# Kernel optimization log

Hardware: AMD Instinct MI355X
Metric: run time of the kernel (lower is better)

The kernel has to match this reference:

```python
import jax, jax.numpy as jnp
import numpy as np
from jax import lax

V, D, H, B, S = 30000, 300, 300, 512, 100
DA, WIND1, HOPS, NC = 100, 40, 3, 7


def setup_inputs() -> dict:
    key = jax.random.key(0)
    ks = iter(jax.random.split(key, 64))
    def w(shape, fan_in):
        return jax.random.normal(next(ks), shape, jnp.float32) / np.float32(np.sqrt(fan_in))
    inp = {}
    inp["sents"] = jax.random.randint(next(ks), (B, S), 0, V)
    inp["lengths"] = jax.random.randint(next(ks), (B,), 1, S + 1)
    inp["emb"] = w((V, D), D)
    for d in ("f", "b"):
        inp["lstm_Wih_" + d] = w((4 * H, D), D)
        inp["lstm_Whh_" + d] = w((4 * H, H), H)
        inp["lstm_bih_" + d] = w((4 * H,), H)
        inp["lstm_bhh_" + d] = w((4 * H,), H)
        inp["gru_Wih_" + d] = w((3 * DA, DA), DA)
        inp["gru_Whh_" + d] = w((3 * DA, DA), DA)
        inp["gru_bih_" + d] = w((3 * DA,), DA)
        inp["gru_bhh_" + d] = w((3 * DA,), DA)
    inp["lin1_W"] = w((DA, 2 * H), 2 * H)
    inp["lin1_b"] = w((DA,), 2 * H)
    for nm in ("att_Wr", "att_Ur", "att_W", "att_U"):
        inp[nm] = w((HOPS, DA, DA), DA)
    for nm in ("att_br", "att_bur", "att_bw", "att_bu"):
        inp[nm] = w((HOPS, DA), DA)
    inp["cls_W"] = w((NC, DA), DA)
    inp["cls_b"] = w((NC,), DA)
    return inp


def _lstm_dir(x_tm, m_tm, Wih, Whh, bih, bhh):
    # x_tm: [S,B,D], m_tm: [S,B,1] bool. Masked scan == pack_padded semantics
    xg = jnp.einsum('sbd,gd->sbg', x_tm, Wih) + bih  # precompute input gates [S,B,4H]
    Hh = Whh.shape[1]
    def step(carry, inp):
        h, c = carry
        xgt, mt = inp
        g = xgt + h @ Whh.T + bhh
        i, f, gg, o = jnp.split(g, 4, -1)  # torch LSTM gate order i,f,g,o
        cn = jax.nn.sigmoid(f) * c + jax.nn.sigmoid(i) * jnp.tanh(gg)
        hn = jax.nn.sigmoid(o) * jnp.tanh(cn)
        return (jnp.where(mt, hn, h), jnp.where(mt, cn, c)), jnp.where(mt, hn, 0.0)
    init = (jnp.zeros((x_tm.shape[1], Hh), x_tm.dtype), jnp.zeros((x_tm.shape[1], Hh), x_tm.dtype))
    _, out = lax.scan(step, init, (xg, m_tm))
    return out


def _gru_dir(x_tm, Wih, Whh, bih, bhh):
    xg = jnp.einsum('sbd,gd->sbg', x_tm, Wih) + bih  # [S,B,3H]
    Hh = Whh.shape[1]
    def step(h, xgt):
        hg = h @ Whh.T + bhh
        xr, xz, xn = jnp.split(xgt, 3, -1)
        hr, hz, hn = jnp.split(hg, 3, -1)
        r = jax.nn.sigmoid(xr + hr)
        z = jax.nn.sigmoid(xz + hz)
        n = jnp.tanh(xn + r * hn)
        h2 = (1.0 - z) * n + z * h
        return h2, h2
    _, out = lax.scan(step, jnp.zeros((x_tm.shape[1], Hh), x_tm.dtype), xg)
    return out


def _attgru(mem_tm, gates_tm, Wr, br, Ur, bur, W, bw, U, bu):
    # mem_tm: [W,B-1,100], gates_tm: [W,B-1,1]; AttnGRUCell recurrence
    cr = jnp.einsum('sbd,hd->sbh', mem_tm, Wr) + br
    cw = jnp.einsum('sbd,hd->sbh', mem_tm, W) + bw
    def step(h, inp):
        crt, cwt, g = inp
        r = jax.nn.sigmoid(crt + h @ Ur.T + bur)
        ht = jnp.tanh(cwt + r * (h @ U.T + bu))
        return g * ht + (1.0 - g) * h, None
    h0 = jnp.zeros((mem_tm.shape[1], Wr.shape[0]), mem_tm.dtype)
    h, _ = lax.scan(step, h0, (cr, cw, gates_tm))
    return h  # [B-1,100]


def reference(sents, lengths, emb,
              lstm_Wih_f, lstm_Whh_f, lstm_bih_f, lstm_bhh_f,
              lstm_Wih_b, lstm_Whh_b, lstm_bih_b, lstm_bhh_b,
              lin1_W, lin1_b,
              gru_Wih_f, gru_Whh_f, gru_bih_f, gru_bhh_f,
              gru_Wih_b, gru_Whh_b, gru_bih_b, gru_bhh_b,
              att_Wr, att_br, att_Ur, att_bur, att_W, att_bw, att_U, att_bu,
              cls_W, cls_b):
    we = emb[sents]  # [B,S,D]
    mask = jnp.arange(S)[None, :] < lengths[:, None]  # [B,S]
    x_tm = we.transpose(1, 0, 2)
    m_tm = mask.T[:, :, None]
    out_f = _lstm_dir(x_tm, m_tm, lstm_Wih_f, lstm_Whh_f, lstm_bih_f, lstm_bhh_f)
    out_b = jnp.flip(_lstm_dir(jnp.flip(x_tm, 0), jnp.flip(m_tm, 0),
                               lstm_Wih_b, lstm_Whh_b, lstm_bih_b, lstm_bhh_b), 0)
    w_gru = jnp.concatenate([out_f, out_b], -1).transpose(1, 0, 2)  # [B,S,2H], 0 at pads
    maxpl = jnp.max(w_gru, axis=1)
    s_utt = jnp.tanh(maxpl @ lin1_W.T + lin1_b)  # [B,100]; dropout = eval identity
    # context window: slot j of query i holds utterance i-WIND1+j (zero-padded front)
    idx = jnp.arange(1, B)[:, None] - WIND1 + jnp.arange(WIND1)[None, :]  # [B-1,W]
    valid = idx >= 0
    bt = s_utt[jnp.clip(idx, 0)] * valid[..., None].astype(s_utt.dtype)  # [B-1,W,100]
    bt_tm = bt.transpose(1, 0, 2)  # [W,B-1,100]
    mem_f = _gru_dir(bt_tm, gru_Wih_f, gru_Whh_f, gru_bih_f, gru_bhh_f)
    mem_b = jnp.flip(_gru_dir(jnp.flip(bt_tm, 0), gru_Wih_b, gru_Whh_b, gru_bih_b, gru_bhh_b), 0)
    mem_tm = bt_tm + mem_f + mem_b  # fusion: input + fwd + bwd GRU states
    mem_bank = mem_tm.transpose(1, 0, 2)  # [B-1,W,100]
    eps = s_utt[1:][:, None, :]  # query [B-1,1,100]
    attn_ws = []
    for hop in range(HOPS):
        attn = jnp.einsum('bqd,bkd->bqk', eps, mem_bank)  # [B-1,1,W]
        attn = jnp.where(valid[:, None, :], attn, -1e10)
        scores = jax.nn.softmax(attn, -1)
        gates_tm = scores[:, 0, :].T[:, :, None]  # [W,B-1,1]
        h = _attgru(mem_tm, gates_tm, att_Wr[hop], att_br[hop], att_Ur[hop], att_bur[hop],
                    att_W[hop], att_bw[hop], att_U[hop], att_bu[hop])
        eps = eps + h[:, None, :]
        attn_ws.append(scores[:, 0, :])
    s_cont = jnp.concatenate([s_utt[:1], eps[:, 0, :]], 0)  # [B,100]
    pred = jax.nn.log_softmax(s_cont @ cls_W.T + cls_b, -1)  # [B,NC]
    return pred, jnp.stack(attn_ws)  # attn weights [HOPS,B-1,W]
```

## Files before the change

### kernel.cpp

```cpp
#include <hip/hip_runtime.h>
#include <cstdint>
#include <cstddef>

typedef unsigned short u16;
typedef unsigned int   u32;
typedef unsigned long long u64;

#define S_LEN 100
#define B_SZ  512
#define H_LS  300
#define NHOP  3
#define NC_   7
#define BM1   511
#define NBD3  60

using bf16x8 = __attribute__((ext_vector_type(8))) short;
using f32x4  = __attribute__((ext_vector_type(4))) float;

__device__ __forceinline__ float u2f(u16 u) {
  union { u32 i; float f; } x; x.i = ((u32)u) << 16; return x.f;
}
__device__ __forceinline__ u16 f2u(float f) {
  u32 bits = __float_as_uint(f);
  bits += 0x7fffu + ((bits >> 16) & 1u);
  return (u16)(bits >> 16);
}
__device__ __forceinline__ float sigm(float x) { return 1.0f / (1.0f + expf(-x)); }

__global__ void detect_k(const u32* __restrict__ raw, int* __restrict__ flag) {
  __shared__ int cnt;
  if (threadIdx.x == 0) cnt = 0;
  __syncthreads();
  u32 w = raw[threadIdx.x];
  u32 lo = w & 0xFFFFu;
  int e = (int)((lo >> 7) & 0xFF);
  int pl = (lo == 0u || (e >= 0x70 && e <= 0x8E)) ? 1 : 0;
  atomicAdd(&cnt, pl);
  __syncthreads();
  if (threadIdx.x == 0) *flag = (cnt >= 192) ? 1 : 0;
}

#define NF_NSEG 28
#define NF_TOT  1748007
struct NormFArgs { const void* src[NF_NSEG]; const int* flag; float* dst; };

__global__ __launch_bounds__(256) void norm_f32(NormFArgs a) {
  const int P[NF_NSEG + 1] = {
    0,360000,720000,1080000,1440000,1441200,1442400,1443600,
    1444800,1474800,1504800,1505100,1505400,1535400,1565400,1565700,
    1566000,1626000,1626100,1656100,1686100,1716100,1746100,1746400,
    1746700,1747000,1747300,1748000,1748007};
  int fl = *a.flag;
  int stride = gridDim.x * 256;
  for (int i = blockIdx.x * 256 + threadIdx.x; i < NF_TOT; i += stride) {
    int s = 0;
    while (i >= P[s + 1]) ++s;
    int k = i - P[s];
    float v = fl ? u2f(((const u16*)a.src[s])[k]) : ((const float*)a.src[s])[k];
    a.dst[i] = v;
  }
}
#define AF_LWIH_F 0
#define AF_LWHH_F 360000
#define AF_LWIH_B 720000
#define AF_LWHH_B 1080000
#define AF_LBIH_F 1440000
#define AF_LBHH_F 1441200
#define AF_LBIH_B 1442400
#define AF_LBHH_B 1443600
#define AF_GWIH_F 1444800
#define AF_GWHH_F 1474800
#define AF_GBIH_F 1504800
#define AF_GBHH_F 1505100
#define AF_GWIH_B 1505400
#define AF_GWHH_B 1535400
#define AF_GBIH_B 1565400
#define AF_GBHH_B 1565700
#define AF_LIN1W  1566000
#define AF_LIN1B  1626000
#define AF_ATTWR  1626100
#define AF_ATTUR  1656100
#define AF_ATTW   1686100
#define AF_ATTU   1716100
#define AF_ATTBR  1746100
#define AF_ATTBUR 1746400
#define AF_ATTBW  1746700
#define AF_ATTBU  1747000
#define AF_CLSW   1747300
#define AF_CLSB   1748000

__global__ void transp_k(const float* __restrict__ allf, float* __restrict__ wt) {
  int idx = blockIdx.x * 256 + threadIdx.x;
  if (idx >= 120000) return;
  int seg = idx / 10000;
  int rem = idx - seg * 10000;
  int k = rem / 100, j = rem - (rem / 100) * 100;
  int srcbase;
  if (seg < 3)      srcbase = AF_GWHH_F + seg * 10000;
  else if (seg < 6) srcbase = AF_GWHH_B + (seg - 3) * 10000;
  else if (seg < 9) srcbase = AF_ATTUR + (seg - 6) * 10000;
  else              srcbase = AF_ATTU  + (seg - 9) * 10000;
  wt[seg * 10000 + k * 100 + j] = allf[srcbase + j * 100 + k];
}

__global__ void tr_lstm2(const float* __restrict__ allf, u16* __restrict__ wL2,
                         float* __restrict__ bsum) {
  int idx = blockIdx.x * 256 + threadIdx.x;
  if (idx < 1536000) {
    int dir = idx / 768000;
    int rem = idx - dir * 768000;
    int c = rem / 640, kp = rem - (rem / 640) * 640;
    int j = c >> 2, g = c & 3;
    float v = 0.f;
    if (kp < 320) {
      if (kp < 300)
        v = allf[(dir ? AF_LWIH_B : AF_LWIH_F) + (g * 300 + j) * 300 + kp];
    } else {
      int k2 = kp - 320;
      if (k2 < 300)
        v = allf[(dir ? AF_LWHH_B : AF_LWHH_F) + (g * 300 + j) * 300 + k2];
    }
    wL2[idx] = f2u(v);
  } else if (idx < 1538400) {
    int i2 = idx - 1536000;
    int dir = i2 / 1200, gj = i2 - (i2 / 1200) * 1200;
    bsum[i2] = allf[(dir ? AF_LBIH_B : AF_LBIH_F) + gj]
             + allf[(dir ? AF_LBHH_B : AF_LBHH_F) + gj];
  }
}

__global__ __launch_bounds__(256) void xgat2(const int* __restrict__ sents,
                                             const void* __restrict__ emb,
                                             const int* __restrict__ flag,
                                             u16* __restrict__ xallR) {
  __shared__ int toks[64];
  int tid = threadIdx.x;
  int r0 = blockIdx.x * 64, t = blockIdx.y;
  int fl = *flag;
  if (tid < 64) toks[tid] = sents[(r0 + tid) * S_LEN + t];
  __syncthreads();
  for (int idx = tid; idx < 64 * 320; idx += 256) {
    int r = idx / 320, k = idx - (idx / 320) * 320;
    u16 v = 0;
    if (k < 300) {
      size_t si = (size_t)toks[r] * 300 + k;
      v = fl ? ((const u16*)emb)[si] : f2u(((const float*)emb)[si]);
    }
    xallR[((size_t)t * 512 + r0 + r) * 320 + k] = v;
  }
}

struct Lstm8Args {
  const int* lens;
  const u16* xallR;
  const u16* wL2;
  const float* bsum;
  float* hbufR;
  float* maxb;
  int* cnt;
};

__global__ __launch_bounds__(512, 1) void lstm8(Lstm8Args a) {
  __shared__ u16   WLh[80 * 640];
  __shared__ float Gs[128][84];
  const int tid = threadIdx.x;
  const int r0  = blockIdx.x * 128;
  const int ct  = blockIdx.y;
  const int dir = blockIdx.z;

  {
    const u64* wsrc = (const u64*)(a.wL2 + (size_t)dir * 768000 + (size_t)ct * 80 * 640);
    for (int i = tid; i < 80 * 160; i += 512) {
      int cc = i / 160, kw = i - (i / 160) * 160;
      u64 v = wsrc[(size_t)cc * 160 + kw];
      *(u64*)((char*)WLh + cc * 1280 + ((kw * 8) ^ ((cc & 7) << 4))) = v;
    }
  }

  const int w  = tid >> 6;
  const int l  = tid & 63;
  const int lr = l & 15;
  const int aq = l >> 4;
  const int arow = r0 + w * 16 + lr;

  float cq[5], hq[5], mxv[5], bsv[5][4];
  int lenv[5];
  #pragma unroll
  for (int i = 0; i < 5; ++i) {
    int idx = tid * 5 + i;
    int r = idx / 20, jj = idx - (idx / 20) * 20;
    int j = ct * 20 + jj;
    cq[i] = 0.f; hq[i] = 0.f; mxv[i] = -INFINITY;
    lenv[i] = a.lens[r0 + r];
    #pragma unroll
    for (int g = 0; g < 4; ++g) bsv[i][g] = a.bsum[dir * 1200 + g * 300 + j];
  }

  int* cptr = a.cnt + dir * 16;
  int target = 0;
  __syncthreads();

  for (int s = 0; s < S_LEN; ++s) {
    const int tt  = dir ? (S_LEN - 1 - s) : s;
    const int cur = s & 1, nxt = cur ^ 1;

    f32x4 acc0 = {0,0,0,0}, acc1 = {0,0,0,0}, acc2 = {0,0,0,0},
          acc3 = {0,0,0,0}, acc4 = {0,0,0,0};

    const u16*   xrow = a.xallR + ((size_t)tt * 512 + arow) * 320 + aq * 8;
    const float* hrow = a.hbufR + (((size_t)cur * 2 + dir) * 512 + arow) * 320 + aq * 8;

    for (int ks = 0; ks < 10; ++ks) {
      bf16x8 Af = *(const bf16x8*)(xrow + ks * 32);
      #pragma unroll
      for (int cf = 0; cf < 5; ++cf) {
        int cc = cf * 16 + lr;
        bf16x8 Bf = *(const bf16x8*)((const char*)WLh + cc * 1280 +
                                     ((ks * 64 + aq * 16) ^ ((cc & 7) << 4)));
        f32x4& ac = (cf == 0) ? acc0 : (cf == 1) ? acc1 : (cf == 2) ? acc2
                  : (cf == 3) ? acc3 : acc4;
        ac = __builtin_amdgcn_mfma_f32_16x16x32_bf16(Af, Bf, ac, 0, 0, 0);
      }
    }
    for (int ks = 0; ks < 10; ++ks) {
      const float* hp = hrow + ks * 32;
      float4 h0 = *(const float4*)hp;
      float4 h1 = *(const float4*)(hp + 4);
      union { u32 u[4]; bf16x8 v; } pk;
      pk.u[0] = ((u32)f2u(h0.y) << 16) | (u32)f2u(h0.x);
      pk.u[1] = ((u32)f2u(h0.w) << 16) | (u32)f2u(h0.z);
      pk.u[2] = ((u32)f2u(h1.y) << 16) | (u32)f2u(h1.x);
      pk.u[3] = ((u32)f2u(h1.w) << 16) | (u32)f2u(h1.z);
      bf16x8 Af = pk.v;
      #pragma unroll
      for (int cf = 0; cf < 5; ++cf) {
        int cc = cf * 16 + lr;
        bf16x8 Bf = *(const bf16x8*)((const char*)WLh + cc * 1280 +
                                     (((ks + 10) * 64 + aq * 16) ^ ((cc & 7) << 4)));
        f32x4& ac = (cf == 0) ? acc0 : (cf == 1) ? acc1 : (cf == 2) ? acc2
                  : (cf == 3) ? acc3 : acc4;
        ac = __builtin_amdgcn_mfma_f32_16x16x32_bf16(Af, Bf, ac, 0, 0, 0);
      }
    }

    #pragma unroll
    for (int rr = 0; rr < 4; ++rr) {
      Gs[w * 16 + aq * 4 + rr][0 * 16 + lr] = acc0[rr];
      Gs[w * 16 + aq * 4 + rr][1 * 16 + lr] = acc1[rr];
      Gs[w * 16 + aq * 4 + rr][2 * 16 + lr] = acc2[rr];
      Gs[w * 16 + aq * 4 + rr][3 * 16 + lr] = acc3[rr];
      Gs[w * 16 + aq * 4 + rr][4 * 16 + lr] = acc4[rr];
    }
    __syncthreads();

    #pragma unroll
    for (int i = 0; i < 5; ++i) {
      int idx = tid * 5 + i;
      int r = idx / 20, jj = idx - (idx / 20) * 20;
      bool m = tt < lenv[i];
      float4 g4 = *(const float4*)&Gs[r][jj * 4];
      if (m) {
        float gi = g4.x + bsv[i][0];
        float gf = g4.y + bsv[i][1];
        float gg = g4.z + bsv[i][2];
        float go = g4.w + bsv[i][3];
        cq[i] = sigm(gf) * cq[i] + sigm(gi) * tanhf(gg);
        hq[i] = sigm(go) * tanhf(cq[i]);
        mxv[i] = fmaxf(mxv[i], hq[i]);
      } else {
        mxv[i] = fmaxf(mxv[i], 0.f);
      }
      a.hbufR[(((size_t)nxt * 2 + dir) * 512 + r0 + r) * 320 + ct * 20 + jj] = hq[i];
    }

    target += NBD3;
    __syncthreads();
    if (tid == 0) {
      __threadfence();
      __hip_atomic_fetch_add(cptr, 1, __ATOMIC_ACQ_REL, __HIP_MEMORY_SCOPE_AGENT);
      while (__hip_atomic_load(cptr, __ATOMIC_ACQUIRE, __HIP_MEMORY_SCOPE_AGENT) < target) {
        __builtin_amdgcn_s_sleep(1);
      }
      __threadfence();
    }
    __syncthreads();
  }

  #pragma unroll
  for (int i = 0; i < 5; ++i) {
    int idx = tid * 5 + i;
    int r = idx / 20, jj = idx - (idx / 20) * 20;
    a.maxb[(size_t)(r0 + r) * 600 + dir * 300 + ct * 20 + jj] = mxv[i];
  }
}

__global__ __launch_bounds__(128) void sutt_k(const float* __restrict__ maxb,
                                              const float* __restrict__ W,
                                              const float* __restrict__ bb,
                                              float* __restrict__ sutt) {
  int b = blockIdx.x, tid = threadIdx.x;
  __shared__ float mx[600];
  for (int i = tid; i < 600; i += 128) mx[i] = maxb[b * 600 + i];
  __syncthreads();
  if (tid < 100) {
    float acc = bb[tid];
    const float* wr = W + tid * 600;
    for (int k = 0; k < 600; ++k) acc += mx[k] * wr[k];
    sutt[b * 100 + tid] = tanhf(acc);
  }
}

__global__ __launch_bounds__(256) void gxg3(const float* __restrict__ sutt,
                                            const float* __restrict__ Wf, const float* __restrict__ bf_,
                                            const float* __restrict__ Wb, const float* __restrict__ bb_,
                                            float* __restrict__ xg) {
  __shared__ float bts[32][101];
  int tid = threadIdx.x;
  int rt = blockIdx.x * 32, t = blockIdx.y, dir = blockIdx.z;
  int tin = dir ? (39 - t) : t;
  for (int idx = tid; idx < 3200; idx += 256) {
    int r = idx / 100, k = idx - r * 100, row = rt + r;
    float v = 0.f;
    if (row < BM1) {
      int srow = row + 1 - 40 + tin;
      if (srow >= 0) v = sutt[srow * 100 + k];
    }
    bts[r][k] = v;
  }
  __syncthreads();
  const float* Wm = dir ? Wb : Wf;
  const float* bm = dir ? bb_ : bf_;
  for (int o = tid; o < 9600; o += 256) {
    int r = o & 31, g = o >> 5;
    float acc = bm[g];
    const float* wr = Wm + g * 100;
    const float* br = bts[r];
    for (int k = 0; k < 100; ++k) acc += br[k] * wr[k];
    int row = rt + r;
    if (row < BM1) xg[(((size_t)dir * 40 + t) * BM1 + row) * 300 + g] = acc;
  }
}

struct Gru4Args {
  const float* wt;
  const float* bhh[2];
  const float* xg;
  float* memf; float* memb;
};

__global__ __launch_bounds__(512) void gru4(Gru4Args a) {
  __shared__ float WT[30000];
  __shared__ float hl[2][4][104];
  int tid = threadIdx.x, rt = blockIdx.x * 4, dir = blockIdx.y;
  const float* src = a.wt + dir * 30000;
  for (int i = tid; i < 30000; i += 512) WT[i] = src[i];
  for (int i = tid; i < 832; i += 512) ((float*)hl)[i] = 0.f;
  int r = tid / 100, j = tid - r * 100;
  int row = rt + r;
  bool act = (tid < 400) && (row < BM1);
  const float* bhh = a.bhh[dir];
  float xr = 0.f, xz = 0.f, xn = 0.f;
  if (act) {
    size_t xb = ((size_t)(dir * 40) * BM1 + row) * 300;
    xr = a.xg[xb + j]; xz = a.xg[xb + 100 + j]; xn = a.xg[xb + 200 + j];
  }
  float hprev = 0.f;
  __syncthreads();
  for (int t = 0; t < 40; ++t) {
    int nxt = (t + 1) & 1, cur = t & 1;
    float xr2 = 0.f, xz2 = 0.f, xn2 = 0.f;
    if (act && t < 39) {
      size_t xb = ((size_t)(dir * 40 + t + 1) * BM1 + row) * 300;
      xr2 = a.xg[xb + j]; xz2 = a.xg[xb + 100 + j]; xn2 = a.xg[xb + 200 + j];
    }
    float v = 0.f;
    if (act) {
      float hr = bhh[j], hz = bhh[100 + j], hn = bhh[200 + j];
      const float* w0 = WT + j;
      const float* hrow = hl[cur][r];
      for (int k = 0; k < 100; ++k) {
        float hv = hrow[k];
        hr += hv * w0[k * 100];
        hz += hv * w0[10000 + k * 100];
        hn += hv * w0[20000 + k * 100];
      }
      float rg_ = sigm(xr + hr), zg = sigm(xz + hz);
      float ng = tanhf(xn + rg_ * hn);
      v = (1.f - zg) * ng + zg * hprev;
      int tin = dir ? (39 - t) : t;
      (dir ? a.memb : a.memf)[((size_t)tin * BM1 + row) * 100 + j] = v;
    }
    if (tid < 400) hl[nxt][r][j] = v;
    hprev = v;
    __syncthreads();
    xr = xr2; xz = xz2; xn = xn2;
  }
}

__global__ void memcomb(const float* __restrict__ memf, const float* __restrict__ memb,
                        const float* __restrict__ sutt, float* __restrict__ memm) {
  int idx = blockIdx.x * 256 + threadIdx.x;
  if (idx >= 40 * BM1 * 100) return;
  int j = idx % 100; int rem = idx / 100; int row = rem % BM1; int t = rem / BM1;
  float v = memf[idx] + memb[idx];
  int sidx = row + 1 - 40 + t;
  if (sidx >= 0) v += sutt[sidx * 100 + j];
  memm[idx] = v;
}

__global__ void epsinit(const float* __restrict__ sutt, float* __restrict__ eps) {
  int idx = blockIdx.x * 256 + threadIdx.x;
  if (idx < BM1 * 100) eps[idx] = sutt[idx + 100];
}

__global__ __launch_bounds__(64) void attnsc(const float* __restrict__ eps,
                                             const float* __restrict__ memm,
                                             float* __restrict__ gatesw,
                                             float* __restrict__ outat) {
  int row = blockIdx.x, k = threadIdx.x;
  __shared__ float el[100];
  for (int i = k; i < 100; i += 64) el[i] = eps[row * 100 + i];
  __syncthreads();
  float val = -INFINITY;
  if (k < 40) {
    if (row + 1 - 40 + k >= 0) {
      const float* mrow = memm + ((size_t)k * BM1 + row) * 100;
      float s = 0.f;
      for (int d = 0; d < 100; ++d) s += el[d] * mrow[d];
      val = s;
    } else val = -1e10f;
  }
  float mx = val;
  for (int off = 32; off > 0; off >>= 1) mx = fmaxf(mx, __shfl_xor(mx, off));
  float ex = (k < 40) ? expf(val - mx) : 0.f;
  float sm = ex;
  for (int off = 32; off > 0; off >>= 1) sm += __shfl_xor(sm, off);
  if (k < 40) {
    float sc = ex / sm;
    gatesw[k * BM1 + row] = sc;
    outat[row * 40 + k] = sc;
  }
}

__global__ __launch_bounds__(256) void crcw3(const float* __restrict__ memm,
                                             const float* __restrict__ Wr, const float* __restrict__ br,
                                             const float* __restrict__ Ww, const float* __restrict__ bw,
                                             float* __restrict__ crb, float* __restrict__ cwb) {
  __shared__ float ml[32][101];
  int tid = threadIdx.x;
  int rt = blockIdx.x * 32, t = blockIdx.y, which = blockIdx.z;
  for (int idx = tid; idx < 3200; idx += 256) {
    int r = idx / 100, k = idx - r * 100; int row = rt + r;
    ml[r][k] = (row < BM1) ? memm[((size_t)t * BM1 + row) * 100 + k] : 0.f;
  }
  __syncthreads();
  const float* Wm = which ? Ww : Wr;
  const float* bm = which ? bw : br;
  float* ob = which ? cwb : crb;
  for (int o = tid; o < 3200; o += 256) {
    int r = o & 31, hh = o >> 5;
    float acc = bm[hh];
    const float* wr = Wm + hh * 100;
    for (int k = 0; k < 100; ++k) acc += ml[r][k] * wr[k];
    int row = rt + r;
    if (row < BM1) ob[((size_t)t * BM1 + row) * 100 + hh] = acc;
  }
}

struct Att4Args {
  const float* urT; const float* uT;
  const float* bur; const float* bu;
  const float* crb; const float* cwb;
  const float* gatesw; float* eps;
};

__global__ __launch_bounds__(512) void attscan4(Att4Args a) {
  __shared__ float UrT[10000];
  __shared__ float UT[10000];
  __shared__ float hl[2][4][104];
  int tid = threadIdx.x, rt = blockIdx.x * 4;
  for (int i = tid; i < 10000; i += 512) { UrT[i] = a.urT[i]; UT[i] = a.uT[i]; }
  for (int i = tid; i < 832; i += 512) ((float*)hl)[i] = 0.f;
  int r = tid / 100, j = tid - r * 100;
  int row = rt + r;
  bool act = (tid < 400) && (row < BM1);
  float cr = 0.f, cw = 0.f, gw = 0.f;
  if (act) {
    size_t ix = (size_t)row * 100 + j;
    cr = a.crb[ix]; cw = a.cwb[ix]; gw = a.gatesw[row];
  }
  float hprev = 0.f;
  __syncthreads();
  for (int t = 0; t < 40; ++t) {
    int nxt = (t + 1) & 1, cur = t & 1;
    float cr2 = 0.f, cw2 = 0.f, gw2 = 0.f;
    if (act && t < 39) {
      size_t ix = ((size_t)(t + 1) * BM1 + row) * 100 + j;
      cr2 = a.crb[ix]; cw2 = a.cwb[ix]; gw2 = a.gatesw[(t + 1) * BM1 + row];
    }
    float v = 0.f;
    if (act) {
      float hr = a.bur[j], hu = a.bu[j];
      const float* hrow = hl[cur][r];
      for (int k = 0; k < 100; ++k) {
        float hv = hrow[k];
        hr += hv * UrT[k * 100 + j];
        hu += hv * UT[k * 100 + j];
      }
      float rg_ = sigm(cr + hr);
      float ht = tanhf(cw + rg_ * hu);
      v = gw * ht + (1.f - gw) * hprev;
    }
    if (tid < 400) hl[nxt][r][j] = v;
    hprev = v;
    __syncthreads();
    cr = cr2; cw = cw2; gw = gw2;
  }
  if (act) a.eps[(size_t)row * 100 + j] += hprev;
}

__global__ __launch_bounds__(64) void cls_k(const float* __restrict__ sutt,
                                            const float* __restrict__ eps,
                                            const float* __restrict__ cW, const float* __restrict__ cb,
                                            float* __restrict__ outp) {
  int b = blockIdx.x, j = threadIdx.x;
  __shared__ float sl[100];
  for (int i = j; i < 100; i += 64) sl[i] = (b == 0) ? sutt[i] : eps[(b - 1) * 100 + i];
  __syncthreads();
  float lg = -INFINITY;
  if (j < 7) {
    lg = cb[j];
    const float* wr = cW + j * 100;
    for (int k = 0; k < 100; ++k) lg += sl[k] * wr[k];
  }
  float mx = lg;
  for (int off = 32; off > 0; off >>= 1) mx = fmaxf(mx, __shfl_xor(mx, off));
  float ex = (j < 7) ? expf(lg - mx) : 0.f;
  float sm = ex;
  for (int off = 32; off > 0; off >>= 1) sm += __shfl_xor(sm, off);
  if (j < 7) outp[b * 7 + j] = lg - mx - logf(sm);
}

extern "C" void kernel_launch(void* const* d_in, const int* in_sizes, int n_in,
                              void* d_out, int out_size, void* d_ws, size_t ws_size,
                              hipStream_t stream) {
  (void)n_in; (void)out_size; (void)ws_size;

  bool sigOrder = (in_sizes[7] == 360000);

  const void *p_sents, *p_lens, *p_emb;
  const void *p_lWih_f, *p_lWhh_f, *p_lbih_f, *p_lbhh_f;
  const void *p_lWih_b, *p_lWhh_b, *p_lbih_b, *p_lbhh_b;
  const void *p_gWih_f, *p_gWhh_f, *p_gbih_f, *p_gbhh_f;
  const void *p_gWih_b, *p_gWhh_b, *p_gbih_b, *p_gbhh_b;
  const void *p_lin1W, *p_lin1b;
  const void *p_attWr, *p_attUr, *p_attW, *p_attU;
  const void *p_attbr, *p_attbur, *p_attbw, *p_attbu;
  const void *p_clsW, *p_clsb;

  p_sents = d_in[0]; p_lens = d_in[1]; p_emb = d_in[2];
  p_lWih_f = d_in[3]; p_lWhh_f = d_in[4]; p_lbih_f = d_in[5]; p_lbhh_f = d_in[6];
  if (sigOrder) {
    p_lWih_b = d_in[7];  p_lWhh_b = d_in[8];  p_lbih_b = d_in[9];  p_lbhh_b = d_in[10];
    p_lin1W  = d_in[11]; p_lin1b  = d_in[12];
    p_gWih_f = d_in[13]; p_gWhh_f = d_in[14]; p_gbih_f = d_in[15]; p_gbhh_f = d_in[16];
    p_gWih_b = d_in[17]; p_gWhh_b = d_in[18]; p_gbih_b = d_in[19]; p_gbhh_b = d_in[20];
    p_attWr  = d_in[21]; p_attbr  = d_in[22]; p_attUr  = d_in[23]; p_attbur = d_in[24];
    p_attW   = d_in[25]; p_attbw  = d_in[26]; p_attU   = d_in[27]; p_attbu  = d_in[28];
    p_clsW   = d_in[29]; p_clsb   = d_in[30];
  } else {
    p_gWih_f = d_in[7];  p_gWhh_f = d_in[8];  p_gbih_f = d_in[9];  p_gbhh_f = d_in[10];
    p_lWih_b = d_in[11]; p_lWhh_b = d_in[12]; p_lbih_b = d_in[13]; p_lbhh_b = d_in[14];
    p_gWih_b = d_in[15]; p_gWhh_b = d_in[16]; p_gbih_b = d_in[17]; p_gbhh_b = d_in[18];
    p_lin1W  = d_in[19]; p_lin1b  = d_in[20];
    p_attWr  = d_in[21]; p_attUr  = d_in[22]; p_attW   = d_in[23]; p_attU   = d_in[24];
    p_attbr  = d_in[25]; p_attbur = d_in[26]; p_attbw  = d_in[27]; p_attbu  = d_in[28];
    p_clsW   = d_in[29]; p_clsb   = d_in[30];
  }

  char* wp = (char*)d_ws;
  auto carve = [&](size_t bytes) {
    char* p = wp;
    wp += (bytes + 255) & ~(size_t)255;
    return p;
  };
  int*   flag  = (int*)  carve(256);
  int*   cnt   = (int*)  carve(256);
  float* allf  = (float*)carve((size_t)NF_TOT * 4);
  float* wt    = (float*)carve((size_t)120000 * 4);
  u16*   wL2   = (u16*)  carve((size_t)1536000 * 2);
  float* bsum  = (float*)carve((size_t)2400 * 4);
  float* hbufR = (float*)carve((size_t)2 * 2 * 512 * 320 * 4);
  float* maxb  = (float*)carve((size_t)B_SZ * 600 * 4);
  float* sutt  = (float*)carve((size_t)B_SZ * 100 * 4);
  size_t xg_sz   = (size_t)2 * 40 * BM1 * 300 * 4;
  size_t memf_sz = (size_t)40 * BM1 * 100 * 4;
  char*  big   = carve(xg_sz + 2 * memf_sz);
  u16*   xallR = (u16*)big;
  float* xg    = (float*)big;
  float* memf  = (float*)(big + xg_sz);
  float* memb  = (float*)(big + xg_sz + memf_sz);
  float* memm  = (float*)carve(memf_sz);
  float* gatesw= (float*)carve((size_t)40 * BM1 * 4);
  float* eps   = (float*)carve((size_t)BM1 * 100 * 4);
  float* crb   = xg;
  float* cwb   = xg + (size_t)40 * BM1 * 100;

  float* out_pred = (float*)d_out;
  float* out_attn = out_pred + (size_t)B_SZ * NC_;

  detect_k<<<1, 256, 0, stream>>>((const u32*)p_emb, flag);

  NormFArgs nf;
  {
    const void* srcs[NF_NSEG] = {
      p_lWih_f, p_lWhh_f, p_lWih_b, p_lWhh_b,
      p_lbih_f, p_lbhh_f, p_lbih_b, p_lbhh_b,
      p_gWih_f, p_gWhh_f, p_gbih_f, p_gbhh_f,
      p_gWih_b, p_gWhh_b, p_gbih_b, p_gbhh_b,
      p_lin1W,  p_lin1b,
      p_attWr,  p_attUr,  p_attW,   p_attU,
      p_attbr,  p_attbur, p_attbw,  p_attbu,
      p_clsW,   p_clsb };
    for (int i = 0; i < NF_NSEG; ++i) nf.src[i] = srcs[i];
    nf.flag = flag; nf.dst = allf;
  }
  norm_f32<<<2048, 256, 0, stream>>>(nf);
  transp_k<<<(120000 + 255) / 256, 256, 0, stream>>>(allf, wt);
  tr_lstm2<<<(1538400 + 255) / 256, 256, 0, stream>>>(allf, wL2, bsum);
  xgat2<<<dim3(8, 100), 256, 0, stream>>>((const int*)p_sents, p_emb, flag, xallR);

  hipMemsetAsync(cnt, 0, 256, stream);
  hipMemsetAsync(hbufR, 0, (size_t)2 * 2 * 512 * 320 * 4, stream);

  Lstm8Args la;
  la.lens = (const int*)p_lens;
  la.xallR = xallR; la.wL2 = wL2; la.bsum = bsum;
  la.hbufR = hbufR; la.maxb = maxb; la.cnt = cnt;
  lstm8<<<dim3(4, 15, 2), 512, 0, stream>>>(la);

  sutt_k<<<512, 128, 0, stream>>>(maxb, allf + AF_LIN1W, allf + AF_LIN1B, sutt);

  gxg3<<<dim3(16, 40, 2), 256, 0, stream>>>(sutt,
      allf + AF_GWIH_F, allf + AF_GBIH_F,
      allf + AF_GWIH_B, allf + AF_GBIH_B, xg);

  Gru4Args ga;
  ga.wt = wt;
  ga.bhh[0] = allf + AF_GBHH_F; ga.bhh[1] = allf + AF_GBHH_B;
  ga.xg = xg; ga.memf = memf; ga.memb = memb;
  gru4<<<dim3(128, 2), 512, 0, stream>>>(ga);

  memcomb<<<(40 * BM1 * 100 + 255) / 256, 256, 0, stream>>>(memf, memb, sutt, memm);
  epsinit<<<(BM1 * 100 + 255) / 256, 256, 0, stream>>>(sutt, eps);

  for (int hop = 0; hop < NHOP; ++hop) {
    attnsc<<<BM1, 64, 0, stream>>>(eps, memm, gatesw, out_attn + (size_t)hop * BM1 * 40);
    crcw3<<<dim3(16, 40, 2), 256, 0, stream>>>(memm,
        allf + AF_ATTWR + hop * 10000, allf + AF_ATTBR + hop * 100,
        allf + AF_ATTW  + hop * 10000, allf + AF_ATTBW + hop * 100, crb, cwb);
    Att4Args aa;
    aa.urT = wt + 60000 + hop * 10000;
    aa.uT  = wt + 90000 + hop * 10000;
    aa.bur = allf + AF_ATTBUR + hop * 100;
    aa.bu  = allf + AF_ATTBU  + hop * 100;
    aa.crb = crb; aa.cwb = cwb;
    aa.gatesw = gatesw; aa.eps = eps;
    attscan4<<<128, 512, 0, stream>>>(aa);
  }

  cls_k<<<512, 64, 0, stream>>>(sutt, eps, allf + AF_CLSW, allf + AF_CLSB, out_pred);
}
```

Measured before the change: 3.218 ms.

## Split LSTM recurrence across twice the blocks with K-split waves and flag barrier

The persistent LSTM kernel now covers 64 batch rows per block instead of 128, doubling the grid to 240 blocks. Within each block, half the waves compute the input-projection GEMM and the other half the recurrent-hidden GEMM, and the two partial sums are reduced through shared memory. The grid barrier changes from every block polling a counter to the last arriver publishing a step flag that the others poll. It also prefetches A operands one k-step ahead. The aim is to shorten the serial per-step critical path across more CUs, at the cost of an extra shared-memory reduction and sync and a larger grid barrier.

```diff
diff --git a/kernel.cpp b/kernel.cpp
--- a/kernel.cpp
+++ b/kernel.cpp
@@ -12,7 +12,7 @@
 #define NHOP  3
 #define NC_   7
 #define BM1   511
-#define NBD3  60
+#define NBD4  120
 
 using bf16x8 = __attribute__((ext_vector_type(8))) short;
 using f32x4  = __attribute__((ext_vector_type(4))) float;
@@ -150,7 +150,7 @@
   }
 }
 
-struct Lstm8Args {
+struct Lstm9Args {
   const int* lens;
   const u16* xallR;
   const u16* wL2;
@@ -160,11 +160,11 @@
   int* cnt;
 };
 
-__global__ __launch_bounds__(512, 1) void lstm8(Lstm8Args a) {
+__global__ __launch_bounds__(512, 1) void lstm9(Lstm9Args a) {
   __shared__ u16   WLh[80 * 640];
-  __shared__ float Gs[128][84];
+  __shared__ float Gs[64 * 85];
   const int tid = threadIdx.x;
-  const int r0  = blockIdx.x * 128;
+  const int r0  = blockIdx.x * 64;
   const int ct  = blockIdx.y;
   const int dir = blockIdx.z;
 
@@ -178,26 +178,34 @@
   }
 
   const int w  = tid >> 6;
+  const int rf = w & 3;
+  const int kh = w >> 2;
   const int l  = tid & 63;
   const int lr = l & 15;
   const int aq = l >> 4;
-  const int arow = r0 + w * 16 + lr;
-
-  float cq[5], hq[5], mxv[5], bsv[5][4];
-  int lenv[5];
+  const int arow = r0 + rf * 16 + lr;
+
+  float cq[3] = {0.f, 0.f, 0.f}, hq[3] = {0.f, 0.f, 0.f};
+  float mxv[3] = {-INFINITY, -INFINITY, -INFINITY};
+  float bsv[3][4];
+  int lenv[3];
   #pragma unroll
-  for (int i = 0; i < 5; ++i) {
-    int idx = tid * 5 + i;
-    int r = idx / 20, jj = idx - (idx / 20) * 20;
-    int j = ct * 20 + jj;
-    cq[i] = 0.f; hq[i] = 0.f; mxv[i] = -INFINITY;
-    lenv[i] = a.lens[r0 + r];
-    #pragma unroll
-    for (int g = 0; g < 4; ++g) bsv[i][g] = a.bsum[dir * 1200 + g * 300 + j];
-  }
-
-  int* cptr = a.cnt + dir * 16;
-  int target = 0;
+  for (int i = 0; i < 3; ++i) {
+    int idx = tid + i * 512;
+    if (idx < 1280) {
+      int r = idx / 20, jj = idx - (idx / 20) * 20;
+      int j = ct * 20 + jj;
+      lenv[i] = a.lens[r0 + r];
+      #pragma unroll
+      for (int g = 0; g < 4; ++g) bsv[i][g] = a.bsum[dir * 1200 + g * 300 + j];
+    } else {
+      lenv[i] = 0;
+      bsv[i][0] = bsv[i][1] = bsv[i][2] = bsv[i][3] = 0.f;
+    }
+  }
+
+  int* cptr = a.cnt + dir * 32;
+  int* fptr = a.cnt + dir * 32 + 16;
   __syncthreads();
 
   for (int s = 0; s < S_LEN; ++s) {
@@ -207,79 +215,108 @@
     f32x4 acc0 = {0,0,0,0}, acc1 = {0,0,0,0}, acc2 = {0,0,0,0},
           acc3 = {0,0,0,0}, acc4 = {0,0,0,0};
 
-    const u16*   xrow = a.xallR + ((size_t)tt * 512 + arow) * 320 + aq * 8;
-    const float* hrow = a.hbufR + (((size_t)cur * 2 + dir) * 512 + arow) * 320 + aq * 8;
-
-    for (int ks = 0; ks < 10; ++ks) {
-      bf16x8 Af = *(const bf16x8*)(xrow + ks * 32);
+    if (kh == 0) {
+      const u16* xrow = a.xallR + ((size_t)tt * 512 + arow) * 320 + aq * 8;
+      bf16x8 Af = *(const bf16x8*)(xrow);
       #pragma unroll
-      for (int cf = 0; cf < 5; ++cf) {
-        int cc = cf * 16 + lr;
-        bf16x8 Bf = *(const bf16x8*)((const char*)WLh + cc * 1280 +
-                                     ((ks * 64 + aq * 16) ^ ((cc & 7) << 4)));
-        f32x4& ac = (cf == 0) ? acc0 : (cf == 1) ? acc1 : (cf == 2) ? acc2
-                  : (cf == 3) ? acc3 : acc4;
-        ac = __builtin_amdgcn_mfma_f32_16x16x32_bf16(Af, Bf, ac, 0, 0, 0);
+      for (int ks = 0; ks < 10; ++ks) {
+        bf16x8 An = (ks < 9) ? *(const bf16x8*)(xrow + (ks + 1) * 32) : Af;
+        #pragma unroll
+        for (int cf = 0; cf < 5; ++cf) {
+          int cc = cf * 16 + lr;
+          bf16x8 Bf = *(const bf16x8*)((const char*)WLh + cc * 1280 +
+                                       ((ks * 64 + aq * 16) ^ ((cc & 7) << 4)));
+          f32x4& ac = (cf == 0) ? acc0 : (cf == 1) ? acc1 : (cf == 2) ? acc2
+                    : (cf == 3) ? acc3 : acc4;
+          ac = __builtin_amdgcn_mfma_f32_16x16x32_bf16(Af, Bf, ac, 0, 0, 0);
+        }
+        Af = An;
       }
-    }
-    for (int ks = 0; ks < 10; ++ks) {
-      const float* hp = hrow + ks * 32;
-      float4 h0 = *(const float4*)hp;
-      float4 h1 = *(const float4*)(hp + 4);
-      union { u32 u[4]; bf16x8 v; } pk;
-      pk.u[0] = ((u32)f2u(h0.y) << 16) | (u32)f2u(h0.x);
-      pk.u[1] = ((u32)f2u(h0.w) << 16) | (u32)f2u(h0.z);
-      pk.u[2] = ((u32)f2u(h1.y) << 16) | (u32)f2u(h1.x);
-      pk.u[3] = ((u32)f2u(h1.w) << 16) | (u32)f2u(h1.z);
-      bf16x8 Af = pk.v;
+    } else {
+      const float* hrow = a.hbufR + (((size_t)cur * 2 + dir) * 512 + arow) * 320 + aq * 8;
+      float4 h0 = *(const float4*)hrow;
+      float4 h1 = *(const float4*)(hrow + 4);
       #pragma unroll
-      for (int cf = 0; cf < 5; ++cf) {
-        int cc = cf * 16 + lr;
-        bf16x8 Bf = *(const bf16x8*)((const char*)WLh + cc * 1280 +
-                                     (((ks + 10) * 64 + aq * 16) ^ ((cc & 7) << 4)));
-        f32x4& ac = (cf == 0) ? acc0 : (cf == 1) ? acc1 : (cf == 2) ? acc2
-                  : (cf == 3) ? acc3 : acc4;
-        ac = __builtin_amdgcn_mfma_f32_16x16x32_bf16(Af, Bf, ac, 0, 0, 0);
+      for (int ks = 0; ks < 10; ++ks) {
+        float4 n0, n1;
+        if (ks < 9) {
+          n0 = *(const float4*)(hrow + (ks + 1) * 32);
+          n1 = *(const float4*)(hrow + (ks + 1) * 32 + 4);
+        }
+        union { u32 u[4]; bf16x8 v; } pk;
+        pk.u[0] = ((u32)f2u(h0.y) << 16) | (u32)f2u(h0.x);
+        pk.u[1] = ((u32)f2u(h0.w) << 16) | (u32)f2u(h0.z);
+        pk.u[2] = ((u32)f2u(h1.y) << 16) | (u32)f2u(h1.x);
+        pk.u[3] = ((u32)f2u(h1.w) << 16) | (u32)f2u(h1.z);
+        bf16x8 Af = pk.v;
+        #pragma unroll
+        for (int cf = 0; cf < 5; ++cf) {
+          int cc = cf * 16 + lr;
+          bf16x8 Bf = *(const bf16x8*)((const char*)WLh + cc * 1280 +
+                                       (((ks + 10) * 64 + aq * 16) ^ ((cc & 7) << 4)));
+          f32x4& ac = (cf == 0) ? acc0 : (cf == 1) ? acc1 : (cf == 2) ? acc2
+                    : (cf == 3) ? acc3 : acc4;
+          ac = __builtin_amdgcn_mfma_f32_16x16x32_bf16(Af, Bf, ac, 0, 0, 0);
+        }
+        if (ks < 9) { h0 = n0; h1 = n1; }
       }
     }
 
+    if (kh == 0) {
+      #pragma unroll
+      for (int rr = 0; rr < 4; ++rr) {
+        int gr = (rf * 16 + aq * 4 + rr) * 85;
+        Gs[gr + 0 * 16 + lr] = acc0[rr];
+        Gs[gr + 1 * 16 + lr] = acc1[rr];
+        Gs[gr + 2 * 16 + lr] = acc2[rr];
+        Gs[gr + 3 * 16 + lr] = acc3[rr];
+        Gs[gr + 4 * 16 + lr] = acc4[rr];
+      }
+    }
+    __syncthreads();
+    if (kh == 1) {
+      #pragma unroll
+      for (int rr = 0; rr < 4; ++rr) {
+        int gr = (rf * 16 + aq * 4 + rr) * 85;
+        Gs[gr + 0 * 16 + lr] += acc0[rr];
+        Gs[gr + 1 * 16 + lr] += acc1[rr];
+        Gs[gr + 2 * 16 + lr] += acc2[rr];
+        Gs[gr + 3 * 16 + lr] += acc3[rr];
+        Gs[gr + 4 * 16 + lr] += acc4[rr];
+      }
+    }
+    __syncthreads();
+
     #pragma unroll
-    for (int rr = 0; rr < 4; ++rr) {
-      Gs[w * 16 + aq * 4 + rr][0 * 16 + lr] = acc0[rr];
-      Gs[w * 16 + aq * 4 + rr][1 * 16 + lr] = acc1[rr];
-      Gs[w * 16 + aq * 4 + rr][2 * 16 + lr] = acc2[rr];
-      Gs[w * 16 + aq * 4 + rr][3 * 16 + lr] = acc3[rr];
-      Gs[w * 16 + aq * 4 + rr][4 * 16 + lr] = acc4[rr];
-    }
-    __syncthreads();
-
-    #pragma unroll
-    for (int i = 0; i < 5; ++i) {
-      int idx = tid * 5 + i;
-      int r = idx / 20, jj = idx - (idx / 20) * 20;
-      bool m = tt < lenv[i];
-      float4 g4 = *(const float4*)&Gs[r][jj * 4];
-      if (m) {
-        float gi = g4.x + bsv[i][0];
-        float gf = g4.y + bsv[i][1];
-        float gg = g4.z + bsv[i][2];
-        float go = g4.w + bsv[i][3];
-        cq[i] = sigm(gf) * cq[i] + sigm(gi) * tanhf(gg);
-        hq[i] = sigm(go) * tanhf(cq[i]);
-        mxv[i] = fmaxf(mxv[i], hq[i]);
-      } else {
-        mxv[i] = fmaxf(mxv[i], 0.f);
+    for (int i = 0; i < 3; ++i) {
+      int idx = tid + i * 512;
+      if (idx < 1280) {
+        int r = idx / 20, jj = idx - (idx / 20) * 20;
+        bool m = tt < lenv[i];
+        if (m) {
+          float gi = Gs[r * 85 + jj * 4 + 0] + bsv[i][0];
+          float gf = Gs[r * 85 + jj * 4 + 1] + bsv[i][1];
+          float gg = Gs[r * 85 + jj * 4 + 2] + bsv[i][2];
+          float go = Gs[r * 85 + jj * 4 + 3] + bsv[i][3];
+          cq[i] = sigm(gf) * cq[i] + sigm(gi) * tanhf(gg);
+          hq[i] = sigm(go) * tanhf(cq[i]);
+          mxv[i] = fmaxf(mxv[i], hq[i]);
+        } else {
+          mxv[i] = fmaxf(mxv[i], 0.f);
+        }
+        a.hbufR[(((size_t)nxt * 2 + dir) * 512 + r0 + r) * 320 + ct * 20 + jj] = hq[i];
       }
-      a.hbufR[(((size_t)nxt * 2 + dir) * 512 + r0 + r) * 320 + ct * 20 + jj] = hq[i];
-    }
-
-    target += NBD3;
+    }
+
     __syncthreads();
     if (tid == 0) {
       __threadfence();
-      __hip_atomic_fetch_add(cptr, 1, __ATOMIC_ACQ_REL, __HIP_MEMORY_SCOPE_AGENT);
-      while (__hip_atomic_load(cptr, __ATOMIC_ACQUIRE, __HIP_MEMORY_SCOPE_AGENT) < target) {
-        __builtin_amdgcn_s_sleep(1);
+      int old = __hip_atomic_fetch_add(cptr, 1, __ATOMIC_ACQ_REL, __HIP_MEMORY_SCOPE_AGENT);
+      if (old == NBD4 * (s + 1) - 1) {
+        __hip_atomic_store(fptr, s + 1, __ATOMIC_RELEASE, __HIP_MEMORY_SCOPE_AGENT);
+      } else {
+        while (__hip_atomic_load(fptr, __ATOMIC_ACQUIRE, __HIP_MEMORY_SCOPE_AGENT) < s + 1)
+          __builtin_amdgcn_s_sleep(2);
       }
       __threadfence();
     }
@@ -287,10 +324,12 @@
   }
 
   #pragma unroll
-  for (int i = 0; i < 5; ++i) {
-    int idx = tid * 5 + i;
-    int r = idx / 20, jj = idx - (idx / 20) * 20;
-    a.maxb[(size_t)(r0 + r) * 600 + dir * 300 + ct * 20 + jj] = mxv[i];
+  for (int i = 0; i < 3; ++i) {
+    int idx = tid + i * 512;
+    if (idx < 1280) {
+      int r = idx / 20, jj = idx - (idx / 20) * 20;
+      a.maxb[(size_t)(r0 + r) * 600 + dir * 300 + ct * 20 + jj] = mxv[i];
+    }
   }
 }
 
@@ -633,11 +672,11 @@
   hipMemsetAsync(cnt, 0, 256, stream);
   hipMemsetAsync(hbufR, 0, (size_t)2 * 2 * 512 * 320 * 4, stream);
 
-  Lstm8Args la;
+  Lstm9Args la;
   la.lens = (const int*)p_lens;
   la.xallR = xallR; la.wL2 = wL2; la.bsum = bsum;
   la.hbufR = hbufR; la.maxb = maxb; la.cnt = cnt;
-  lstm8<<<dim3(4, 15, 2), 512, 0, stream>>>(la);
+  lstm9<<<dim3(8, 15, 2), 512, 0, stream>>>(la);
 
   sutt_k<<<512, 128, 0, stream>>>(maxb, allf + AF_LIN1W, allf + AF_LIN1B, sutt);
 
```

Result: slower. 3.941 ms (+22.5%).

## Make LSTM blocks own batch rows so the recurrence needs no grid barrier

Applied to the files above, without the earlier changes.

The LSTM kernel is reorganised so that each block handles 16 batch rows and all 1200 gate columns for one direction, which replaces the 120-block column-split design. The hidden state then stays in shared memory as bf16, so the per-step global atomic spin barrier and the global h buffer round trip are removed. The cost is that weights can no longer sit in LDS: every block streams the full 1.5 MB per-direction weight matrix from global memory or L2 at every timestep, and only 64 blocks are launched. Whether L2 bandwidth can keep up with this weight streaming decides the outcome.

```diff
diff --git a/kernel.cpp b/kernel.cpp
--- a/kernel.cpp
+++ b/kernel.cpp
@@ -12,7 +12,6 @@
 #define NHOP  3
 #define NC_   7
 #define BM1   511
-#define NBD3  60
 
 using bf16x8 = __attribute__((ext_vector_type(8))) short;
 using f32x4  = __attribute__((ext_vector_type(4))) float;
@@ -150,147 +149,113 @@
   }
 }
 
-struct Lstm8Args {
+struct Lstm12Args {
   const int* lens;
   const u16* xallR;
   const u16* wL2;
   const float* bsum;
-  float* hbufR;
   float* maxb;
-  int* cnt;
 };
 
-__global__ __launch_bounds__(512, 1) void lstm8(Lstm8Args a) {
-  __shared__ u16   WLh[80 * 640];
-  __shared__ float Gs[128][84];
+__global__ __launch_bounds__(512, 1) void lstm12(Lstm12Args a) {
+  __shared__ u16 hL[2][16 * 320];
   const int tid = threadIdx.x;
-  const int r0  = blockIdx.x * 128;
-  const int ct  = blockIdx.y;
-  const int dir = blockIdx.z;
-
-  {
-    const u64* wsrc = (const u64*)(a.wL2 + (size_t)dir * 768000 + (size_t)ct * 80 * 640);
-    for (int i = tid; i < 80 * 160; i += 512) {
-      int cc = i / 160, kw = i - (i / 160) * 160;
-      u64 v = wsrc[(size_t)cc * 160 + kw];
-      *(u64*)((char*)WLh + cc * 1280 + ((kw * 8) ^ ((cc & 7) << 4))) = v;
-    }
-  }
-
-  const int w  = tid >> 6;
-  const int l  = tid & 63;
-  const int lr = l & 15;
-  const int aq = l >> 4;
-  const int arow = r0 + w * 16 + lr;
-
-  float cq[5], hq[5], mxv[5], bsv[5][4];
-  int lenv[5];
+  const int r0  = blockIdx.x * 16;
+  const int dir = blockIdx.y;
+  const int w   = tid >> 6;
+  const int l   = tid & 63;
+  const int lr  = l & 15;
+  const int aq  = l >> 4;
+  const int row = r0 + lr;
+  const int len = a.lens[row];
+
+  const int cfStart = (w < 3) ? w * 10 : 30 + (w - 3) * 9;
+  const int cfCount = (w < 3) ? 10 : 9;
+
+  for (int i = tid; i < 16 * 320; i += 512) { hL[0][i] = 0; hL[1][i] = 0; }
+
+  float bs[10][4];
   #pragma unroll
-  for (int i = 0; i < 5; ++i) {
-    int idx = tid * 5 + i;
-    int r = idx / 20, jj = idx - (idx / 20) * 20;
-    int j = ct * 20 + jj;
-    cq[i] = 0.f; hq[i] = 0.f; mxv[i] = -INFINITY;
-    lenv[i] = a.lens[r0 + r];
+  for (int i = 0; i < 10; ++i) {
+    bool va = (i < cfCount);
+    int j = va ? ((cfStart + i) * 4 + aq) : 0;
     #pragma unroll
-    for (int g = 0; g < 4; ++g) bsv[i][g] = a.bsum[dir * 1200 + g * 300 + j];
-  }
-
-  int* cptr = a.cnt + dir * 16;
-  int target = 0;
+    for (int g = 0; g < 4; ++g)
+      bs[i][g] = va ? a.bsum[dir * 1200 + g * 300 + j] : 0.f;
+  }
+  float cq[10], mxv[10];
+  #pragma unroll
+  for (int i = 0; i < 10; ++i) { cq[i] = 0.f; mxv[i] = -INFINITY; }
+
+  const u16* wbase = a.wL2 + (size_t)dir * 768000;
   __syncthreads();
 
   for (int s = 0; s < S_LEN; ++s) {
     const int tt  = dir ? (S_LEN - 1 - s) : s;
     const int cur = s & 1, nxt = cur ^ 1;
-
-    f32x4 acc0 = {0,0,0,0}, acc1 = {0,0,0,0}, acc2 = {0,0,0,0},
-          acc3 = {0,0,0,0}, acc4 = {0,0,0,0};
-
-    const u16*   xrow = a.xallR + ((size_t)tt * 512 + arow) * 320 + aq * 8;
-    const float* hrow = a.hbufR + (((size_t)cur * 2 + dir) * 512 + arow) * 320 + aq * 8;
-
-    for (int ks = 0; ks < 10; ++ks) {
-      bf16x8 Af = *(const bf16x8*)(xrow + ks * 32);
+    const u16* xrow = a.xallR + ((size_t)tt * 512 + row) * 320 + aq * 8;
+    const bool m = tt < len;
+
+    #pragma unroll
+    for (int chunk = 0; chunk < 2; ++chunk) {
+      const int nc = (chunk == 0) ? 5 : (cfCount - 5);
+      f32x4 acc[5];
       #pragma unroll
-      for (int cf = 0; cf < 5; ++cf) {
-        int cc = cf * 16 + lr;
-        bf16x8 Bf = *(const bf16x8*)((const char*)WLh + cc * 1280 +
-                                     ((ks * 64 + aq * 16) ^ ((cc & 7) << 4)));
-        f32x4& ac = (cf == 0) ? acc0 : (cf == 1) ? acc1 : (cf == 2) ? acc2
-                  : (cf == 3) ? acc3 : acc4;
-        ac = __builtin_amdgcn_mfma_f32_16x16x32_bf16(Af, Bf, ac, 0, 0, 0);
+      for (int ci = 0; ci < 5; ++ci) acc[ci] = (f32x4){0, 0, 0, 0};
+
+      for (int ks = 0; ks < 20; ++ks) {
+        bf16x8 Bf;
+        if (ks < 10) {
+          Bf = *(const bf16x8*)(xrow + ks * 32);
+        } else {
+          int kb = (ks - 10) * 64 + aq * 16;
+          Bf = *(const bf16x8*)((const char*)hL[cur] + lr * 640 +
+                                (kb ^ ((lr & 7) << 4)));
+        }
+        #pragma unroll
+        for (int ci = 0; ci < 5; ++ci) {
+          if (ci < nc) {
+            int cc = cfStart + chunk * 5 + ci;
+            bf16x8 Af = *(const bf16x8*)(wbase + (size_t)(cc * 16 + lr) * 640 +
+                                         ks * 32 + aq * 8);
+            acc[ci] = __builtin_amdgcn_mfma_f32_16x16x32_bf16(Af, Bf, acc[ci], 0, 0, 0);
+          }
+        }
       }
-    }
-    for (int ks = 0; ks < 10; ++ks) {
-      const float* hp = hrow + ks * 32;
-      float4 h0 = *(const float4*)hp;
-      float4 h1 = *(const float4*)(hp + 4);
-      union { u32 u[4]; bf16x8 v; } pk;
-      pk.u[0] = ((u32)f2u(h0.y) << 16) | (u32)f2u(h0.x);
-      pk.u[1] = ((u32)f2u(h0.w) << 16) | (u32)f2u(h0.z);
-      pk.u[2] = ((u32)f2u(h1.y) << 16) | (u32)f2u(h1.x);
-      pk.u[3] = ((u32)f2u(h1.w) << 16) | (u32)f2u(h1.z);
-      bf16x8 Af = pk.v;
+
       #pragma unroll
-      for (int cf = 0; cf < 5; ++cf) {
-        int cc = cf * 16 + lr;
-        bf16x8 Bf = *(const bf16x8*)((const char*)WLh + cc * 1280 +
-                                     (((ks + 10) * 64 + aq * 16) ^ ((cc & 7) << 4)));
-        f32x4& ac = (cf == 0) ? acc0 : (cf == 1) ? acc1 : (cf == 2) ? acc2
-                  : (cf == 3) ? acc3 : acc4;
-        ac = __builtin_amdgcn_mfma_f32_16x16x32_bf16(Af, Bf, ac, 0, 0, 0);
+      for (int ci = 0; ci < 5; ++ci) {
+        if (ci < nc) {
+          int idx = chunk * 5 + ci;
+          int j = (cfStart + idx) * 4 + aq;
+          int hbyte = lr * 640 + ((j * 2) ^ ((lr & 7) << 4));
+          u16 hv16;
+          if (m) {
+            float gi_ = acc[ci][0] + bs[idx][0];
+            float gf  = acc[ci][1] + bs[idx][1];
+            float gg  = acc[ci][2] + bs[idx][2];
+            float go  = acc[ci][3] + bs[idx][3];
+            cq[idx] = sigm(gf) * cq[idx] + sigm(gi_) * tanhf(gg);
+            float hn = sigm(go) * tanhf(cq[idx]);
+            mxv[idx] = fmaxf(mxv[idx], hn);
+            hv16 = f2u(hn);
+          } else {
+            mxv[idx] = fmaxf(mxv[idx], 0.f);
+            hv16 = *(const u16*)((const char*)hL[cur] + hbyte);
+          }
+          *(u16*)((char*)hL[nxt] + hbyte) = hv16;
+        }
       }
     }
-
-    #pragma unroll
-    for (int rr = 0; rr < 4; ++rr) {
-      Gs[w * 16 + aq * 4 + rr][0 * 16 + lr] = acc0[rr];
-      Gs[w * 16 + aq * 4 + rr][1 * 16 + lr] = acc1[rr];
-      Gs[w * 16 + aq * 4 + rr][2 * 16 + lr] = acc2[rr];
-      Gs[w * 16 + aq * 4 + rr][3 * 16 + lr] = acc3[rr];
-      Gs[w * 16 + aq * 4 + rr][4 * 16 + lr] = acc4[rr];
-    }
     __syncthreads();
-
-    #pragma unroll
-    for (int i = 0; i < 5; ++i) {
-      int idx = tid * 5 + i;
-      int r = idx / 20, jj = idx - (idx / 20) * 20;
-      bool m = tt < lenv[i];
-      float4 g4 = *(const float4*)&Gs[r][jj * 4];
-      if (m) {
-        float gi = g4.x + bsv[i][0];
-        float gf = g4.y + bsv[i][1];
-        float gg = g4.z + bsv[i][2];
-        float go = g4.w + bsv[i][3];
-        cq[i] = sigm(gf) * cq[i] + sigm(gi) * tanhf(gg);
-        hq[i] = sigm(go) * tanhf(cq[i]);
-        mxv[i] = fmaxf(mxv[i], hq[i]);
-      } else {
-        mxv[i] = fmaxf(mxv[i], 0.f);
-      }
-      a.hbufR[(((size_t)nxt * 2 + dir) * 512 + r0 + r) * 320 + ct * 20 + jj] = hq[i];
-    }
-
-    target += NBD3;
-    __syncthreads();
-    if (tid == 0) {
-      __threadfence();
-      __hip_atomic_fetch_add(cptr, 1, __ATOMIC_ACQ_REL, __HIP_MEMORY_SCOPE_AGENT);
-      while (__hip_atomic_load(cptr, __ATOMIC_ACQUIRE, __HIP_MEMORY_SCOPE_AGENT) < target) {
-        __builtin_amdgcn_s_sleep(1);
-      }
-      __threadfence();
-    }
-    __syncthreads();
   }
 
   #pragma unroll
-  for (int i = 0; i < 5; ++i) {
-    int idx = tid * 5 + i;
-    int r = idx / 20, jj = idx - (idx / 20) * 20;
-    a.maxb[(size_t)(r0 + r) * 600 + dir * 300 + ct * 20 + jj] = mxv[i];
+  for (int i = 0; i < 10; ++i) {
+    if (i < cfCount) {
+      int j = (cfStart + i) * 4 + aq;
+      a.maxb[(size_t)row * 600 + dir * 300 + j] = mxv[i];
+    }
   }
 }
 
@@ -585,12 +550,10 @@
     return p;
   };
   int*   flag  = (int*)  carve(256);
-  int*   cnt   = (int*)  carve(256);
   float* allf  = (float*)carve((size_t)NF_TOT * 4);
   float* wt    = (float*)carve((size_t)120000 * 4);
   u16*   wL2   = (u16*)  carve((size_t)1536000 * 2);
   float* bsum  = (float*)carve((size_t)2400 * 4);
-  float* hbufR = (float*)carve((size_t)2 * 2 * 512 * 320 * 4);
   float* maxb  = (float*)carve((size_t)B_SZ * 600 * 4);
   float* sutt  = (float*)carve((size_t)B_SZ * 100 * 4);
   size_t xg_sz   = (size_t)2 * 40 * BM1 * 300 * 4;
@@ -630,14 +593,11 @@
   tr_lstm2<<<(1538400 + 255) / 256, 256, 0, stream>>>(allf, wL2, bsum);
   xgat2<<<dim3(8, 100), 256, 0, stream>>>((const int*)p_sents, p_emb, flag, xallR);
 
-  hipMemsetAsync(cnt, 0, 256, stream);
-  hipMemsetAsync(hbufR, 0, (size_t)2 * 2 * 512 * 320 * 4, stream);
-
-  Lstm8Args la;
+  Lstm12Args la;
   la.lens = (const int*)p_lens;
   la.xallR = xallR; la.wL2 = wL2; la.bsum = bsum;
-  la.hbufR = hbufR; la.maxb = maxb; la.cnt = cnt;
-  lstm8<<<dim3(4, 15, 2), 512, 0, stream>>>(la);
+  la.maxb = maxb;
+  lstm12<<<dim3(32, 2), 512, 0, stream>>>(la);
 
   sutt_k<<<512, 128, 0, stream>>>(maxb, allf + AF_LIN1W, allf + AF_LIN1B, sutt);
 
```

Measured after the change: 5.775 ms. 79.5% more time.
